# Optimization experiments

Hardware: AMD Instinct MI355X
Metric: run time of the kernel (lower is better)

## Reference

```python
import jax, jax.numpy as jnp
import numpy as np

N, P, C = 100000, 64, 128
DIST_TH = 0.1


def setup_inputs() -> dict:
    key = jax.random.key(0)
    ks = jax.random.split(key, 12)
    xyz = jax.random.uniform(ks[0], (N, 3), jnp.float32) * 10.0  # room coords in [0,10)^3
    feature = jax.random.normal(ks[1], (N, C), jnp.float32)
    center = jax.random.uniform(ks[2], (P, 3), jnp.float32) * 10.0
    normal = jax.random.normal(ks[3], (P, 3), jnp.float32)
    normal = normal / jnp.linalg.norm(normal, axis=1, keepdims=True)
    pmin = center - 1.5  # axis-aligned extent used on axes 0,1
    pmax = center + 1.5
    inp = {
        'feature': feature, 'xyz': xyz,
        'plane_center': center, 'plane_normal': normal,
        'plane_min': pmin, 'plane_max': pmax,
        'W1': jax.random.normal(ks[4], (C, 2 * C), jnp.float32) * (1.0 / np.sqrt(C)),
        's1': jnp.ones((2 * C,), jnp.float32), 'b1': jnp.zeros((2 * C,), jnp.float32),
        'W2': jax.random.normal(ks[5], (2 * C, C), jnp.float32) * (1.0 / np.sqrt(2 * C)),
        's2': jnp.ones((C,), jnp.float32), 'b2': jnp.zeros((C,), jnp.float32),
        'W3': jax.random.normal(ks[6], (C, 1), jnp.float32) * (1.0 / np.sqrt(C)),
        'b3': jnp.zeros((1,), jnp.float32),
        'Wa': jax.random.normal(ks[7], (C, C), jnp.float32) * (1.0 / np.sqrt(C)),
        'Wm': jax.random.normal(ks[8], (C, C), jnp.float32) * (1.0 / np.sqrt(C)),
        'bm': jnp.zeros((C,), jnp.float32),
    }
    return inp


def reference(feature, xyz, plane_center, plane_normal, plane_min, plane_max,
              W1, s1, b1, W2, s2, b2, W3, b3, Wa, Wm, bm):
    # pointwise MLP (shared across planes): fc1 (conv+BN+ReLU), fc2 (conv+BN+ReLU)
    h = jax.nn.relu((feature @ W1) * s1 + b1)          # [N, 2C]
    h2 = jax.nn.relu((h @ W2) * s2 + b2)               # [N, C] == plane_feature
    logit = (h2 @ W3 + b3)[:, 0]                        # [N] fc3 logits (plane_result)

    # per-plane point membership masks (dense [N, P])
    proj = xyz @ plane_normal.T                         # [N, P]
    offs = jnp.sum(plane_center * plane_normal, axis=1) # [P]
    dist_mask = jnp.abs(proj - offs[None, :]) < DIST_TH
    rng = ((xyz[:, None, 0] >= plane_min[None, :, 0]) & (xyz[:, None, 0] < plane_max[None, :, 0]) &
           (xyz[:, None, 1] >= plane_min[None, :, 1]) & (xyz[:, None, 1] < plane_max[None, :, 1]))
    mask = dist_mask & rng                              # [N, P]

    on_sel = jax.nn.sigmoid(logit) > 0.5                # [N]
    on_mask = (mask & on_sel[:, None]).astype(feature.dtype)
    off_mask = (mask & ~on_sel[:, None]).astype(feature.dtype)

    # attention pooling: masked softmax over points, per plane, per channel
    a = h2 @ Wa                                         # [N, C] att activations
    e = jnp.exp(a - jnp.max(a, axis=0, keepdims=True))  # stable exp, [N, C]
    eh = e * h2

    def att_pool(m):                                    # m: [N, P] float
        num = jnp.einsum('np,nc->pc', m, eh)
        den = jnp.einsum('np,nc->pc', m, e)
        agg = num / (den + 1e-9)                        # masked-softmax weighted sum
        return jax.nn.relu(agg @ Wm + bm)               # att_pooling.mlp (conv+ReLU)

    ori = jnp.concatenate([plane_center, plane_normal, plane_min, plane_max], axis=1)  # [P, 12]
    on_feat = jnp.concatenate([att_pool(on_mask), ori], axis=1)    # [P, C+12]
    off_feat = jnp.concatenate([att_pool(off_mask), ori], axis=1)  # [P, C+12]
    return logit, on_feat, off_feat
```

## Files before the change

### kernel.cpp

```cpp
#include <hip/hip_runtime.h>

#define NPTS 100000
#define P 64
#define C 128
#define NBLK 1563
#define BLK_REC 48
#define LIST_CAP 4096
#define CNT_STRIDE 16

typedef __bf16 bf16_t;
typedef __bf16 bf16x8 __attribute__((ext_vector_type(8)));
typedef float floatx4 __attribute__((ext_vector_type(4)));


__global__ __launch_bounds__(256) void prep_kernel(
    const float* __restrict__ W1, const float* __restrict__ s1,
    const float* __restrict__ W2, const float* __restrict__ s2,
    const float* __restrict__ Wa,
    bf16_t* __restrict__ W1t, bf16_t* __restrict__ W2t, bf16_t* __restrict__ Wat,
    unsigned* __restrict__ cnt)
{
  int i0 = blockIdx.x * blockDim.x + threadIdx.x;
  int stride = gridDim.x * blockDim.x;
  for (int i = i0; i < 256 * 128; i += stride) {
    int n = i >> 7, k = i & 127;
    W1t[i] = (bf16_t)(W1[k * 256 + n] * s1[n]);
  }
  for (int i = i0; i < 128 * 256; i += stride) {
    int n = i >> 8, k = i & 255;
    W2t[i] = (bf16_t)(W2[k * 128 + n] * s2[n]);
  }
  for (int i = i0; i < 128 * 128; i += stride) {
    int n = i >> 7, k = i & 127;
    Wat[i] = (bf16_t)(Wa[k * 128 + n]);
  }
  if (i0 < 64 * CNT_STRIDE) cnt[i0] = 0;
}

__global__ __launch_bounds__(256) void main_kernel(
    const float* __restrict__ feature, const float* __restrict__ xyz,
    const float* __restrict__ b1, const float* __restrict__ b2,
    const float* __restrict__ W3, const float* __restrict__ b3,
    const float* __restrict__ ctr, const float* __restrict__ nrm,
    const float* __restrict__ pmn, const float* __restrict__ pmx,
    const bf16_t* __restrict__ W1t, const bf16_t* __restrict__ W2t,
    const bf16_t* __restrict__ Wat,
    unsigned* __restrict__ cnt, unsigned* __restrict__ list,
    bf16_t* __restrict__ rec, float* __restrict__ out_logit)
{
  __shared__ __align__(16) char smem[52752];
  bf16_t* A1   = (bf16_t*)smem;
  bf16_t* Hs   = (bf16_t*)(smem + 17408);
  bf16_t* aB   = (bf16_t*)(smem + 17408);
  float*  w3S  = (float*)(smem + 51200);
  float*  xyzS = (float*)(smem + 51712);
  float*  lgS  = (float*)(smem + 52480);
  unsigned* blkCnt = (unsigned*)(smem + 52736);

  const int tid  = threadIdx.x;
  const int wave = tid >> 6, lane = tid & 63;
  const int quad = lane >> 4, l16 = lane & 15;
  const int m0 = blockIdx.x * 64;

  if (tid < 128) w3S[tid] = W3[tid];
  if (tid < 192) {
    int gi = m0 * 3 + tid;
    xyzS[tid] = (gi < NPTS * 3) ? xyz[gi] : 0.f;
  }
  if (tid == 0) *blkCnt = 0;

  for (int i = tid; i < 64 * 32; i += 256) {
    int r = i >> 5, c4 = i & 31;
    float4 v = make_float4(0.f, 0.f, 0.f, 0.f);
    if (m0 + r < NPTS) v = *(const float4*)(feature + (size_t)(m0 + r) * C + c4 * 4);
    bf16_t* dst = A1 + r * 136 + c4 * 4;
    dst[0] = (bf16_t)v.x; dst[1] = (bf16_t)v.y; dst[2] = (bf16_t)v.z; dst[3] = (bf16_t)v.w;
  }
  __syncthreads();

  const floatx4 zero4 = {0.f, 0.f, 0.f, 0.f};

  {
    floatx4 acc1[4][4];
#pragma unroll
    for (int mt = 0; mt < 4; ++mt)
#pragma unroll
      for (int nt = 0; nt < 4; ++nt) acc1[mt][nt] = zero4;
#pragma unroll
    for (int kt = 0; kt < 4; ++kt) {
      bf16x8 af[4], bfr[4];
#pragma unroll
      for (int mt = 0; mt < 4; ++mt)
        af[mt] = *(const bf16x8*)(A1 + (mt * 16 + l16) * 136 + kt * 32 + quad * 8);
#pragma unroll
      for (int nt = 0; nt < 4; ++nt)
        bfr[nt] = *(const bf16x8*)(W1t + (wave * 64 + nt * 16 + l16) * 128 + kt * 32 + quad * 8);
#pragma unroll
      for (int mt = 0; mt < 4; ++mt)
#pragma unroll
        for (int nt = 0; nt < 4; ++nt)
          acc1[mt][nt] = __builtin_amdgcn_mfma_f32_16x16x32_bf16(af[mt], bfr[nt], acc1[mt][nt], 0, 0, 0);
    }
#pragma unroll
    for (int nt = 0; nt < 4; ++nt) {
      int col = wave * 64 + nt * 16 + l16;
      float bias = b1[col];
#pragma unroll
      for (int mt = 0; mt < 4; ++mt)
#pragma unroll
        for (int r = 0; r < 4; ++r) {
          float hv = fmaxf(acc1[mt][nt][r] + bias, 0.f);
          Hs[(mt * 16 + quad * 4 + r) * 264 + col] = (bf16_t)hv;
        }
    }
  }
  __syncthreads();

  {
    floatx4 acc2[4][2];
#pragma unroll
    for (int mt = 0; mt < 4; ++mt) { acc2[mt][0] = zero4; acc2[mt][1] = zero4; }
#pragma unroll
    for (int kt = 0; kt < 8; ++kt) {
      bf16x8 af[4], bfr[2];
#pragma unroll
      for (int mt = 0; mt < 4; ++mt)
        af[mt] = *(const bf16x8*)(Hs + (mt * 16 + l16) * 264 + kt * 32 + quad * 8);
#pragma unroll
      for (int nt = 0; nt < 2; ++nt)
        bfr[nt] = *(const bf16x8*)(W2t + (wave * 32 + nt * 16 + l16) * 256 + kt * 32 + quad * 8);
#pragma unroll
      for (int mt = 0; mt < 4; ++mt)
#pragma unroll
        for (int nt = 0; nt < 2; ++nt)
          acc2[mt][nt] = __builtin_amdgcn_mfma_f32_16x16x32_bf16(af[mt], bfr[nt], acc2[mt][nt], 0, 0, 0);
    }
#pragma unroll
    for (int nt = 0; nt < 2; ++nt) {
      int col = wave * 32 + nt * 16 + l16;
      float bias = b2[col];
#pragma unroll
      for (int mt = 0; mt < 4; ++mt)
#pragma unroll
        for (int r = 0; r < 4; ++r) {
          float hv = fmaxf(acc2[mt][nt][r] + bias, 0.f);
          A1[(mt * 16 + quad * 4 + r) * 136 + col] = (bf16_t)hv;
        }
    }
  }
  __syncthreads();

  {
    floatx4 acca[4][2];
#pragma unroll
    for (int mt = 0; mt < 4; ++mt) { acca[mt][0] = zero4; acca[mt][1] = zero4; }
#pragma unroll
    for (int kt = 0; kt < 4; ++kt) {
      bf16x8 af[4], bfr[2];
#pragma unroll
      for (int mt = 0; mt < 4; ++mt)
        af[mt] = *(const bf16x8*)(A1 + (mt * 16 + l16) * 136 + kt * 32 + quad * 8);
#pragma unroll
      for (int nt = 0; nt < 2; ++nt)
        bfr[nt] = *(const bf16x8*)(Wat + (wave * 32 + nt * 16 + l16) * 128 + kt * 32 + quad * 8);
#pragma unroll
      for (int mt = 0; mt < 4; ++mt)
#pragma unroll
        for (int nt = 0; nt < 2; ++nt)
          acca[mt][nt] = __builtin_amdgcn_mfma_f32_16x16x32_bf16(af[mt], bfr[nt], acca[mt][nt], 0, 0, 0);
    }
#pragma unroll
    for (int nt = 0; nt < 2; ++nt) {
      int col = wave * 32 + nt * 16 + l16;
#pragma unroll
      for (int mt = 0; mt < 4; ++mt)
#pragma unroll
        for (int r = 0; r < 4; ++r)
          aB[(mt * 16 + quad * 4 + r) * 136 + col] = (bf16_t)acca[mt][nt][r];
    }
  }
  __syncthreads();

  {
    const int m = tid >> 2, g = tid & 3, c0g = g * 32;
    const int mg = m0 + m;
    float lsum = 0.f;
#pragma unroll 8
    for (int c = 0; c < 32; ++c)
      lsum += (float)A1[m * 136 + c0g + c] * w3S[c0g + c];
    lsum += __shfl_xor(lsum, 1);
    lsum += __shfl_xor(lsum, 2);
    if (g == 0) {
      float lg = lsum + b3[0];
      lgS[m] = lg;
      if (mg < NPTS) out_logit[mg] = lg;
    }
  }
  __syncthreads();

  {
    const float nx = nrm[lane * 3], ny = nrm[lane * 3 + 1], nz = nrm[lane * 3 + 2];
    const float offsP = ctr[lane * 3] * nx + ctr[lane * 3 + 1] * ny + ctr[lane * 3 + 2] * nz;
    const float mnx = pmn[lane * 3], mny = pmn[lane * 3 + 1];
    const float mxx = pmx[lane * 3], mxy = pmx[lane * 3 + 1];

    for (int s = 0; s < 16; ++s) {
      const int pt = wave * 16 + s;
      const bool valid = (m0 + pt) < NPTS;
      const float x = xyzS[pt * 3], y = xyzS[pt * 3 + 1], z = xyzS[pt * 3 + 2];
      const float proj = x * nx + y * ny + z * nz;
      const bool hit = valid && (fabsf(proj - offsP) < 0.1f) &&
                       (x >= mnx) && (x < mxx) && (y >= mny) && (y < mxy);
      unsigned long long mball = __ballot(hit);
      if (!mball) continue;

      unsigned slot = 0;
      if (lane == 0) slot = atomicAdd(blkCnt, 1u);
      slot = (unsigned)__shfl((int)slot, 0);
      if (slot >= BLK_REC) continue;

      const unsigned ridx = (unsigned)blockIdx.x * BLK_REC + slot;
      const int sel = (lgS[pt] > 0.f) ? 0 : 1;
      const unsigned ap = ((const unsigned*)(aB + pt * 136))[lane];
      const unsigned hp = ((const unsigned*)(A1 + pt * 136))[lane];
      unsigned* dst = (unsigned*)(rec + (size_t)ridx * 256);
      dst[lane]      = ap;
      dst[64 + lane] = hp;
      if (hit) {
        unsigned idx = atomicAdd(&cnt[lane * CNT_STRIDE], 1u);
        if (idx < LIST_CAP)
          list[lane * LIST_CAP + idx] = (ridx << 1) | (unsigned)sel;
      }
    }
  }
}

__global__ __launch_bounds__(256) void pool2_kernel(
    const unsigned* __restrict__ cnt, const unsigned* __restrict__ list,
    const bf16_t* __restrict__ rec, float* __restrict__ partial)
{
  const int plane = blockIdx.x >> 4;
  const int chunk = blockIdx.x & 15;
  const int tid = threadIdx.x, wave = tid >> 6, lane = tid & 63;

  __shared__ float accS[4][128];
  for (int i = tid; i < 512; i += 256) ((float*)accS)[i] = 0.f;
  __syncthreads();

  unsigned n = cnt[plane * CNT_STRIDE];
  if (n > LIST_CAP) n = LIST_CAP;
  const unsigned* lp = list + plane * LIST_CAP;

  float nOn0 = 0, nOn1 = 0, dOn0 = 0, dOn1 = 0;
  float nOf0 = 0, nOf1 = 0, dOf0 = 0, dOf1 = 0;

  for (unsigned e = (unsigned)(chunk * 4 + wave); e < n; e += 64) {
    const unsigned ent = lp[e];
    const unsigned row = ent >> 1;
    const unsigned* r32 = (const unsigned*)(rec + (size_t)row * 256);
    const unsigned ap = r32[lane];
    const unsigned hp = r32[64 + lane];
    const float a0 = __uint_as_float(ap << 16);
    const float a1 = __uint_as_float(ap & 0xffff0000u);
    const float h0 = __uint_as_float(hp << 16);
    const float h1 = __uint_as_float(hp & 0xffff0000u);
    const float e0 = __expf(a0), e1 = __expf(a1);
    if (!(ent & 1)) { nOn0 += e0 * h0; nOn1 += e1 * h1; dOn0 += e0; dOn1 += e1; }
    else            { nOf0 += e0 * h0; nOf1 += e1 * h1; dOf0 += e0; dOf1 += e1; }
  }

  atomicAdd(&accS[0][lane * 2],     nOn0);
  atomicAdd(&accS[0][lane * 2 + 1], nOn1);
  atomicAdd(&accS[1][lane * 2],     dOn0);
  atomicAdd(&accS[1][lane * 2 + 1], dOn1);
  atomicAdd(&accS[2][lane * 2],     nOf0);
  atomicAdd(&accS[2][lane * 2 + 1], nOf1);
  atomicAdd(&accS[3][lane * 2],     dOf0);
  atomicAdd(&accS[3][lane * 2 + 1], dOf1);
  __syncthreads();

  float* dst = partial + (size_t)blockIdx.x * 512;
  for (int i = tid; i < 512; i += 256) dst[i] = ((float*)accS)[i];
}

__global__ __launch_bounds__(128) void finalize_kernel(
    const float* __restrict__ partial,
    const float* __restrict__ Wm, const float* __restrict__ bm,
    const float* __restrict__ ctr, const float* __restrict__ nrm,
    const float* __restrict__ pmn, const float* __restrict__ pmx,
    float* __restrict__ out)
{
  int sel = blockIdx.x >> 6, p = blockIdx.x & 63;
  int j = threadIdx.x;
  float num = 0.f, den = 0.f;
  const float* bp = partial + (size_t)p * 16 * 512 + sel * 2 * 128;
#pragma unroll
  for (int k = 0; k < 16; ++k) {
    num += bp[k * 512 + j];
    den += bp[k * 512 + 128 + j];
  }
  __shared__ float aggS[128];
  aggS[j] = num / (den + 1e-9f);
  __syncthreads();
  float s = bm[j];
#pragma unroll 4
  for (int c = 0; c < C; ++c) s += aggS[c] * Wm[c * C + j];
  s = fmaxf(s, 0.f);
  float* dst = out + NPTS + sel * (P * 140) + p * 140;
  dst[j] = s;
  if (j < 12) {
    float v;
    if (j < 3)      v = ctr[p * 3 + j];
    else if (j < 6) v = nrm[p * 3 + j - 3];
    else if (j < 9) v = pmn[p * 3 + j - 6];
    else            v = pmx[p * 3 + j - 9];
    dst[C + j] = v;
  }
}

extern "C" void kernel_launch(void* const* d_in, const int* in_sizes, int n_in,
                              void* d_out, int out_size, void* d_ws, size_t ws_size,
                              hipStream_t stream)
{
  const float* feature = (const float*)d_in[0];
  const float* xyz     = (const float*)d_in[1];
  const float* ctr     = (const float*)d_in[2];
  const float* nrm     = (const float*)d_in[3];
  const float* pmn     = (const float*)d_in[4];
  const float* pmx     = (const float*)d_in[5];
  const float* W1      = (const float*)d_in[6];
  const float* s1      = (const float*)d_in[7];
  const float* b1      = (const float*)d_in[8];
  const float* W2      = (const float*)d_in[9];
  const float* s2      = (const float*)d_in[10];
  const float* b2      = (const float*)d_in[11];
  const float* W3      = (const float*)d_in[12];
  const float* b3      = (const float*)d_in[13];
  const float* Wa      = (const float*)d_in[14];
  const float* Wm      = (const float*)d_in[15];
  const float* bm      = (const float*)d_in[16];
  float* out = (float*)d_out;

  char* ws = (char*)d_ws;
  bf16_t*   W1t  = (bf16_t*)(ws);
  bf16_t*   W2t  = (bf16_t*)(ws + 65536);
  bf16_t*   Wat  = (bf16_t*)(ws + 131072);
  unsigned* cnt  = (unsigned*)(ws + 163840);
  unsigned* list = (unsigned*)(ws + 167936);
  bf16_t*   rec  = (bf16_t*)(ws + 1216512);
  float* partial = (float*)(ws + 1216512 + (size_t)NBLK * BLK_REC * 512);

  prep_kernel<<<64, 256, 0, stream>>>(W1, s1, W2, s2, Wa, W1t, W2t, Wat, cnt);
  main_kernel<<<NBLK, 256, 0, stream>>>(
      feature, xyz, b1, b2, W3, b3, ctr, nrm, pmn, pmx,
      W1t, W2t, Wat, cnt, list, rec, out);
  pool2_kernel<<<64 * 16, 256, 0, stream>>>(cnt, list, rec, partial);
  finalize_kernel<<<128, 128, 0, stream>>>(partial, Wm, bm, ctr, nrm, pmn, pmx, out);
}
```

Measured before the change: 194.1 us.

## Split fc1/fc2 into halves to shrink LDS and fuse pooling with finalize

The main kernel now computes the 256-wide hidden layer in two 128-column halves. Each half is consumed into the fc2 accumulators right away, so the hidden staging buffer shrinks from a 264-stride to a 136-stride tile. That cuts shared memory from about 52KB to about 36KB and adds a launch-bounds hint of 4 blocks per CU, to raise occupancy. The pooling and finalize kernels are merged into one kernel with one block per plane, which removes the partial-sum buffer and one launch. The cost is an extra barrier per half in the main kernel and less parallelism in pooling, with 64 blocks instead of 1024.

```diff
diff --git a/kernel.cpp b/kernel.cpp
--- a/kernel.cpp
+++ b/kernel.cpp
@@ -37,7 +37,7 @@
   if (i0 < 64 * CNT_STRIDE) cnt[i0] = 0;
 }
 
-__global__ __launch_bounds__(256) void main_kernel(
+__global__ __launch_bounds__(256, 4) void main_kernel(
     const float* __restrict__ feature, const float* __restrict__ xyz,
     const float* __restrict__ b1, const float* __restrict__ b2,
     const float* __restrict__ W3, const float* __restrict__ b3,
@@ -48,14 +48,14 @@
     unsigned* __restrict__ cnt, unsigned* __restrict__ list,
     bf16_t* __restrict__ rec, float* __restrict__ out_logit)
 {
-  __shared__ __align__(16) char smem[52752];
+  __shared__ __align__(16) char smem[36368];
   bf16_t* A1   = (bf16_t*)smem;
-  bf16_t* Hs   = (bf16_t*)(smem + 17408);
+  bf16_t* Hh   = (bf16_t*)(smem + 17408);
   bf16_t* aB   = (bf16_t*)(smem + 17408);
-  float*  w3S  = (float*)(smem + 51200);
-  float*  xyzS = (float*)(smem + 51712);
-  float*  lgS  = (float*)(smem + 52480);
-  unsigned* blkCnt = (unsigned*)(smem + 52736);
+  float*  w3S  = (float*)(smem + 34816);
+  float*  xyzS = (float*)(smem + 35328);
+  float*  lgS  = (float*)(smem + 36096);
+  unsigned* blkCnt = (unsigned*)(smem + 36352);
 
   const int tid  = threadIdx.x;
   const int wave = tid >> 6, lane = tid & 63;
@@ -80,73 +80,73 @@
 
   const floatx4 zero4 = {0.f, 0.f, 0.f, 0.f};
 
-  {
-    floatx4 acc1[4][4];
-#pragma unroll
-    for (int mt = 0; mt < 4; ++mt)
-#pragma unroll
-      for (int nt = 0; nt < 4; ++nt) acc1[mt][nt] = zero4;
+  floatx4 acc2[4][2];
+#pragma unroll
+  for (int mt = 0; mt < 4; ++mt) { acc2[mt][0] = zero4; acc2[mt][1] = zero4; }
+
+#pragma unroll
+  for (int half = 0; half < 2; ++half) {
+    floatx4 acc1[4][2];
+#pragma unroll
+    for (int mt = 0; mt < 4; ++mt) { acc1[mt][0] = zero4; acc1[mt][1] = zero4; }
 #pragma unroll
     for (int kt = 0; kt < 4; ++kt) {
-      bf16x8 af[4], bfr[4];
+      bf16x8 af[4], bfr[2];
 #pragma unroll
       for (int mt = 0; mt < 4; ++mt)
         af[mt] = *(const bf16x8*)(A1 + (mt * 16 + l16) * 136 + kt * 32 + quad * 8);
 #pragma unroll
-      for (int nt = 0; nt < 4; ++nt)
-        bfr[nt] = *(const bf16x8*)(W1t + (wave * 64 + nt * 16 + l16) * 128 + kt * 32 + quad * 8);
-#pragma unroll
-      for (int mt = 0; mt < 4; ++mt)
-#pragma unroll
-        for (int nt = 0; nt < 4; ++nt)
+      for (int nt = 0; nt < 2; ++nt)
+        bfr[nt] = *(const bf16x8*)(W1t + (size_t)(half * 128 + wave * 32 + nt * 16 + l16) * 128 + kt * 32 + quad * 8);
+#pragma unroll
+      for (int mt = 0; mt < 4; ++mt)
+#pragma unroll
+        for (int nt = 0; nt < 2; ++nt)
           acc1[mt][nt] = __builtin_amdgcn_mfma_f32_16x16x32_bf16(af[mt], bfr[nt], acc1[mt][nt], 0, 0, 0);
     }
 #pragma unroll
-    for (int nt = 0; nt < 4; ++nt) {
-      int col = wave * 64 + nt * 16 + l16;
-      float bias = b1[col];
+    for (int nt = 0; nt < 2; ++nt) {
+      int hcol = wave * 32 + nt * 16 + l16;
+      float bias = b1[half * 128 + hcol];
 #pragma unroll
       for (int mt = 0; mt < 4; ++mt)
 #pragma unroll
         for (int r = 0; r < 4; ++r) {
           float hv = fmaxf(acc1[mt][nt][r] + bias, 0.f);
-          Hs[(mt * 16 + quad * 4 + r) * 264 + col] = (bf16_t)hv;
+          Hh[(mt * 16 + quad * 4 + r) * 136 + hcol] = (bf16_t)hv;
         }
     }
-  }
-  __syncthreads();
-
-  {
-    floatx4 acc2[4][2];
-#pragma unroll
-    for (int mt = 0; mt < 4; ++mt) { acc2[mt][0] = zero4; acc2[mt][1] = zero4; }
-#pragma unroll
-    for (int kt = 0; kt < 8; ++kt) {
+    __syncthreads();
+
+#pragma unroll
+    for (int kt = 0; kt < 4; ++kt) {
       bf16x8 af[4], bfr[2];
 #pragma unroll
       for (int mt = 0; mt < 4; ++mt)
-        af[mt] = *(const bf16x8*)(Hs + (mt * 16 + l16) * 264 + kt * 32 + quad * 8);
+        af[mt] = *(const bf16x8*)(Hh + (mt * 16 + l16) * 136 + kt * 32 + quad * 8);
 #pragma unroll
       for (int nt = 0; nt < 2; ++nt)
-        bfr[nt] = *(const bf16x8*)(W2t + (wave * 32 + nt * 16 + l16) * 256 + kt * 32 + quad * 8);
+        bfr[nt] = *(const bf16x8*)(W2t + (size_t)(wave * 32 + nt * 16 + l16) * 256 + half * 128 + kt * 32 + quad * 8);
 #pragma unroll
       for (int mt = 0; mt < 4; ++mt)
 #pragma unroll
         for (int nt = 0; nt < 2; ++nt)
           acc2[mt][nt] = __builtin_amdgcn_mfma_f32_16x16x32_bf16(af[mt], bfr[nt], acc2[mt][nt], 0, 0, 0);
     }
-#pragma unroll
-    for (int nt = 0; nt < 2; ++nt) {
-      int col = wave * 32 + nt * 16 + l16;
-      float bias = b2[col];
-#pragma unroll
-      for (int mt = 0; mt < 4; ++mt)
-#pragma unroll
-        for (int r = 0; r < 4; ++r) {
-          float hv = fmaxf(acc2[mt][nt][r] + bias, 0.f);
-          A1[(mt * 16 + quad * 4 + r) * 136 + col] = (bf16_t)hv;
-        }
-    }
+    __syncthreads();
+  }
+
+#pragma unroll
+  for (int nt = 0; nt < 2; ++nt) {
+    int col = wave * 32 + nt * 16 + l16;
+    float bias = b2[col];
+#pragma unroll
+    for (int mt = 0; mt < 4; ++mt)
+#pragma unroll
+      for (int r = 0; r < 4; ++r) {
+        float hv = fmaxf(acc2[mt][nt][r] + bias, 0.f);
+        A1[(mt * 16 + quad * 4 + r) * 136 + col] = (bf16_t)hv;
+      }
   }
   __syncthreads();
 
@@ -162,7 +162,7 @@
         af[mt] = *(const bf16x8*)(A1 + (mt * 16 + l16) * 136 + kt * 32 + quad * 8);
 #pragma unroll
       for (int nt = 0; nt < 2; ++nt)
-        bfr[nt] = *(const bf16x8*)(Wat + (wave * 32 + nt * 16 + l16) * 128 + kt * 32 + quad * 8);
+        bfr[nt] = *(const bf16x8*)(Wat + (size_t)(wave * 32 + nt * 16 + l16) * 128 + kt * 32 + quad * 8);
 #pragma unroll
       for (int mt = 0; mt < 4; ++mt)
 #pragma unroll
@@ -235,15 +235,19 @@
   }
 }
 
-__global__ __launch_bounds__(256) void pool2_kernel(
+__global__ __launch_bounds__(256) void poolfin_kernel(
     const unsigned* __restrict__ cnt, const unsigned* __restrict__ list,
-    const bf16_t* __restrict__ rec, float* __restrict__ partial)
+    const bf16_t* __restrict__ rec,
+    const float* __restrict__ Wm, const float* __restrict__ bm,
+    const float* __restrict__ ctr, const float* __restrict__ nrm,
+    const float* __restrict__ pmn, const float* __restrict__ pmx,
+    float* __restrict__ out)
 {
-  const int plane = blockIdx.x >> 4;
-  const int chunk = blockIdx.x & 15;
+  const int plane = blockIdx.x;
   const int tid = threadIdx.x, wave = tid >> 6, lane = tid & 63;
 
   __shared__ float accS[4][128];
+  __shared__ float aggS[2][128];
   for (int i = tid; i < 512; i += 256) ((float*)accS)[i] = 0.f;
   __syncthreads();
 
@@ -254,7 +258,7 @@
   float nOn0 = 0, nOn1 = 0, dOn0 = 0, dOn1 = 0;
   float nOf0 = 0, nOf1 = 0, dOf0 = 0, dOf1 = 0;
 
-  for (unsigned e = (unsigned)(chunk * 4 + wave); e < n; e += 64) {
+  for (unsigned e = (unsigned)wave; e < n; e += 4) {
     const unsigned ent = lp[e];
     const unsigned row = ent >> 1;
     const unsigned* r32 = (const unsigned*)(rec + (size_t)row * 256);
@@ -279,41 +283,23 @@
   atomicAdd(&accS[3][lane * 2 + 1], dOf1);
   __syncthreads();
 
-  float* dst = partial + (size_t)blockIdx.x * 512;
-  for (int i = tid; i < 512; i += 256) dst[i] = ((float*)accS)[i];
-}
-
-__global__ __launch_bounds__(128) void finalize_kernel(
-    const float* __restrict__ partial,
-    const float* __restrict__ Wm, const float* __restrict__ bm,
-    const float* __restrict__ ctr, const float* __restrict__ nrm,
-    const float* __restrict__ pmn, const float* __restrict__ pmx,
-    float* __restrict__ out)
-{
-  int sel = blockIdx.x >> 6, p = blockIdx.x & 63;
-  int j = threadIdx.x;
-  float num = 0.f, den = 0.f;
-  const float* bp = partial + (size_t)p * 16 * 512 + sel * 2 * 128;
-#pragma unroll
-  for (int k = 0; k < 16; ++k) {
-    num += bp[k * 512 + j];
-    den += bp[k * 512 + 128 + j];
-  }
-  __shared__ float aggS[128];
-  aggS[j] = num / (den + 1e-9f);
-  __syncthreads();
+  if (tid < 128) aggS[0][tid] = accS[0][tid] / (accS[1][tid] + 1e-9f);
+  else           aggS[1][tid - 128] = accS[2][tid - 128] / (accS[3][tid - 128] + 1e-9f);
+  __syncthreads();
+
+  const int sel = tid >> 7, j = tid & 127;
   float s = bm[j];
 #pragma unroll 4
-  for (int c = 0; c < C; ++c) s += aggS[c] * Wm[c * C + j];
+  for (int c = 0; c < C; ++c) s += aggS[sel][c] * Wm[c * C + j];
   s = fmaxf(s, 0.f);
-  float* dst = out + NPTS + sel * (P * 140) + p * 140;
+  float* dst = out + NPTS + sel * (P * 140) + plane * 140;
   dst[j] = s;
   if (j < 12) {
     float v;
-    if (j < 3)      v = ctr[p * 3 + j];
-    else if (j < 6) v = nrm[p * 3 + j - 3];
-    else if (j < 9) v = pmn[p * 3 + j - 6];
-    else            v = pmx[p * 3 + j - 9];
+    if (j < 3)      v = ctr[plane * 3 + j];
+    else if (j < 6) v = nrm[plane * 3 + j - 3];
+    else if (j < 9) v = pmn[plane * 3 + j - 6];
+    else            v = pmx[plane * 3 + j - 9];
     dst[C + j] = v;
   }
 }
@@ -348,12 +334,12 @@
   unsigned* cnt  = (unsigned*)(ws + 163840);
   unsigned* list = (unsigned*)(ws + 167936);
   bf16_t*   rec  = (bf16_t*)(ws + 1216512);
-  float* partial = (float*)(ws + 1216512 + (size_t)NBLK * BLK_REC * 512);
 
   prep_kernel<<<64, 256, 0, stream>>>(W1, s1, W2, s2, Wa, W1t, W2t, Wat, cnt);
   main_kernel<<<NBLK, 256, 0, stream>>>(
       feature, xyz, b1, b2, W3, b3, ctr, nrm, pmn, pmx,
       W1t, W2t, Wat, cnt, list, rec, out);
-  pool2_kernel<<<64 * 16, 256, 0, stream>>>(cnt, list, rec, partial);
-  finalize_kernel<<<128, 128, 0, stream>>>(partial, Wm, bm, ctr, nrm, pmn, pmx, out);
+  poolfin_kernel<<<64, 256, 0, stream>>>(
+      cnt, list, rec, Wm, bm, ctr, nrm, pmn, pmx, out);
+  finalize_kernel_unused:;
 }
```

Result: slower. 260.6 us (+34.3%).
